# Kernel optimization log

Measured on AMD Instinct MI355X. Metric: run time of the kernel, lower is better.

Reference implementation:

```python
import jax, jax.numpy as jnp
import numpy as np

IOU_THR = 0.7
SCORE_THR = 0.01
KEEP_TOPK = 300
B, N, C = 16, 2048, 80


def box_cxcywh_to_xyxy(b):
    cx, cy, w, h = b[..., 0], b[..., 1], b[..., 2], b[..., 3]
    return jnp.stack([cx - 0.5 * w, cy - 0.5 * h, cx + 0.5 * w, cy + 0.5 * h], axis=-1)


def _iou_matrix(b):
    # b: [N,4] xyxy -> [N,N] IoU
    area = (b[:, 2] - b[:, 0]) * (b[:, 3] - b[:, 1])
    lt = jnp.maximum(b[:, None, :2], b[None, :, :2])
    rb = jnp.minimum(b[:, None, 2:], b[None, :, 2:])
    wh = jnp.clip(rb - lt, 0.0)
    inter = wh[..., 0] * wh[..., 1]
    union = area[:, None] + area[None, :] - inter
    return jnp.where(union > 0, inter / union, 0.0)


def _nms_image(boxes, scores, labels):
    # boxes [N,4], scores [N], labels [N] -> padded (labels [K], boxes [K,4], scores [K])
    n = boxes.shape[0]
    s = jnp.where(scores > SCORE_THR, scores, -1.0)
    order = jnp.argsort(-s)  # descending score, thresholded-out last
    b = boxes[order]
    sc = s[order]
    lb = labels[order]
    keep0 = sc > SCORE_THR
    # batched_nms trick: offset boxes per class so different classes never overlap
    offset = lb.astype(boxes.dtype) * (jnp.max(boxes) + 1.0)
    iou = _iou_matrix(b + offset[:, None])  # [N,N]
    idxs = jnp.arange(n)

    def body(i, keep):
        sup = keep[i] & (iou[i] > IOU_THR) & (idxs > i)
        return keep & ~sup

    keep = jax.lax.fori_loop(0, n, body, keep0)
    # first KEEP_TOPK kept boxes in score order; pad invalid slots
    sel = jnp.sort(jnp.where(keep, idxs, n))[:KEEP_TOPK]
    ok = sel < n
    sel_c = jnp.minimum(sel, n - 1)
    out_b = jnp.where(ok[:, None], b[sel_c], 0.0)
    out_s = jnp.where(ok, sc[sel_c], 0.0)
    out_l = jnp.where(ok, lb[sel_c], -1)
    return out_l, out_b, out_s


def setup_inputs() -> dict:
    key = jax.random.key(0)
    k1, k2, k3 = jax.random.split(key, 3)
    pred_logits = jax.random.normal(k1, (B, N, C), dtype=jnp.float32)
    pred_boxes = jax.random.uniform(k2, (B, N, 4), dtype=jnp.float32)  # normalized cxcywh
    orig_target_sizes = 480.0 + 800.0 * jax.random.uniform(k3, (B, 2), dtype=jnp.float32)
    return {"pred_logits": pred_logits, "pred_boxes": pred_boxes,
            "orig_target_sizes": orig_target_sizes}


def reference(pred_logits, pred_boxes, orig_target_sizes):
    boxes = box_cxcywh_to_xyxy(pred_boxes)  # [B,N,4]
    scale = jnp.tile(orig_target_sizes, (1, 2))[:, None, :]  # [B,1,4] = (w,h,w,h)
    boxes = boxes * scale
    vals = jnp.max(pred_logits, axis=-1)
    labels = jnp.argmax(pred_logits, axis=-1)
    scores = jax.nn.sigmoid(vals)
    out_l, out_b, out_s = jax.vmap(_nms_image)(boxes, scores, labels)
    return out_l, out_b, out_s
```

## Files before the change

### kernel.cpp

```cpp
#include <hip/hip_runtime.h>


#define NTHREADS 1024
constexpr int Bn = 16;
constexpr int Nn = 2048;
constexpr int Cc = 80;
constexpr int Kk = 300;
constexpr int CCAP = 64;
constexpr double IOU_THR = 0.7;
constexpr double SCORE_THR = 0.01;

__device__ unsigned long long g_keys[Bn * Nn];
__device__ unsigned long long g_skeys[Bn * Nn];
__device__ unsigned char g_lab[Bn * Nn];
__device__ unsigned short g_clp[Bn * Cc * CCAP];
__device__ unsigned short g_cloi[Bn * Cc * CCAP];
__device__ int g_ccnt[Bn * Cc];
__device__ unsigned int g_keepw[Bn * (Nn / 32)];

__global__ __launch_bounds__(256) void argmax_kernel(const float* __restrict__ logits)
{
    int gid = blockIdx.x * 256 + threadIdx.x;
    if (gid >= Bn * Nn) return;
    const float4* lp = (const float4*)(logits + (size_t)gid * Cc);
    float m = -__builtin_inff();
    int am = 0;
#pragma unroll
    for (int c = 0; c < Cc / 4; ++c) {
        float4 v = lp[c];
        if (v.x > m) { m = v.x; am = 4 * c + 0; }
        if (v.y > m) { m = v.y; am = 4 * c + 1; }
        if (v.z > m) { m = v.z; am = 4 * c + 2; }
        if (v.w > m) { m = v.w; am = 4 * c + 3; }
    }
    unsigned mb = __float_as_uint(m);
    unsigned asc = mb ^ ((mb & 0x80000000u) ? 0xFFFFFFFFu : 0x80000000u);
    unsigned n = (unsigned)(gid & (Nn - 1));
    g_keys[gid] = ((unsigned long long)(~asc) << 32) | n;
    g_lab[gid] = (unsigned char)am;
}

__device__ __forceinline__ void cx(unsigned long long& a, unsigned long long p, bool takeMin)
{
    bool aless = a < p;
    a = (takeMin == aless) ? a : p;
}

__launch_bounds__(NTHREADS, 1)
__global__ void sort_compact_kernel()
{
    __shared__ unsigned long long dbuf[2][Nn];
    __shared__ unsigned int hist[32 * Cc];
    __shared__ int s_nv;
    const int t = threadIdx.x;
    const int b = blockIdx.x;
    const size_t base = (size_t)b * Nn;

    if (t == 0) s_nv = 0;
    if (t < Nn / 32) g_keepw[b * (Nn / 32) + t] = 0u;
    for (int i = t; i < 32 * Cc; i += NTHREADS) hist[i] = 0u;

    unsigned long long v0 = g_keys[base + t];
    unsigned long long v1 = g_keys[base + t + 1024];

    {
        int vc = 0;
#pragma unroll
        for (int e = 0; e < 2; ++e) {
            unsigned hi = (unsigned)((e ? v1 : v0) >> 32);
            unsigned ascb = ~hi;
            unsigned mb = (ascb & 0x80000000u) ? (ascb ^ 0x80000000u) : ~ascb;
            float m = __uint_as_float(mb);
            double sd = 1.0 / (1.0 + exp(-(double)m));
            if (sd > SCORE_THR) vc++;
        }
        for (int off = 32; off > 0; off >>= 1) vc += __shfl_down(vc, off);
        if ((t & 63) == 0) atomicAdd(&s_nv, vc);
    }

    int cur = 0;
    for (int k = 2; k <= Nn; k <<= 1) {
        for (int j = k >> 1; j > 0; j >>= 1) {
            if (j >= 1024) {
                unsigned long long mn = (v0 < v1) ? v0 : v1;
                unsigned long long mx = (v0 < v1) ? v1 : v0;
                v0 = mn; v1 = mx;
            } else if (j >= 64) {
                dbuf[cur][t] = v0;
                dbuf[cur][t + 1024] = v1;
                __syncthreads();
                unsigned long long p0 = dbuf[cur][t ^ j];
                unsigned long long p1 = dbuf[cur][(t ^ j) + 1024];
                bool lower = ((t & j) == 0);
                cx(v0, p0, lower == ((t & k) == 0));
                cx(v1, p1, lower == (((t + 1024) & k) == 0));
                cur ^= 1;
            } else {
                unsigned long long p0 = __shfl_xor(v0, j);
                unsigned long long p1 = __shfl_xor(v1, j);
                bool lower = ((t & j) == 0);
                cx(v0, p0, lower == ((t & k) == 0));
                cx(v1, p1, lower == (((t + 1024) & k) == 0));
            }
        }
    }
    const int nv = s_nv;

    const int oi0 = (int)(v0 & 0xFFFFu);
    const int oi1 = (int)(v1 & 0xFFFFu);
    const int c0 = (t < nv) ? (int)g_lab[base + oi0] : 127;
    const int c1 = (t + 1024 < nv) ? (int)g_lab[base + oi1] : 127;
    if (c0 < 127) atomicAdd(&hist[(t >> 6) * Cc + c0], 1u);
    if (c1 < 127) atomicAdd(&hist[((t + 1024) >> 6) * Cc + c1], 1u);
    g_skeys[base + t] = v0;
    g_skeys[base + t + 1024] = v1;
    __syncthreads();

    if (t < Cc) {
        unsigned run = 0;
        for (int ch = 0; ch < 32; ++ch) {
            unsigned v = hist[ch * Cc + t];
            hist[ch * Cc + t] = run;
            run += v;
        }
        g_ccnt[b * Cc + t] = (int)((run < CCAP) ? run : CCAP);
    }
    __syncthreads();

    const int l = t & 63;
    const unsigned long long below = (l == 0) ? 0ull : ((1ull << l) - 1ull);
#pragma unroll
    for (int e = 0; e < 2; ++e) {
        const int p = e ? (t + 1024) : t;
        const int c7 = e ? c1 : c0;
        const int oi = e ? oi1 : oi0;
        unsigned long long mm = ~0ull;
#pragma unroll
        for (int bit = 0; bit < 7; ++bit) {
            unsigned long long vote = __ballot((c7 >> bit) & 1);
            mm &= ((c7 >> bit) & 1) ? vote : ~vote;
        }
        if (c7 < 127) {
            int r = (int)hist[(p >> 6) * Cc + c7] + __popcll(mm & below);
            if (r < CCAP) {
                g_clp[((size_t)b * Cc + c7) * CCAP + r] = (unsigned short)p;
                g_cloi[((size_t)b * Cc + c7) * CCAP + r] = (unsigned short)oi;
            }
        }
    }
}

__launch_bounds__(64, 8)
__global__ void pairnms_kernel(const float* __restrict__ pboxes,
                               const float* __restrict__ osize)
{
    __shared__ double lb[CCAP][5];
    const int bc = blockIdx.x;
    const int b = bc / Cc;
    const int j = threadIdx.x;
    const int cnt = g_ccnt[bc];
    if (cnt == 0) return;
    const double s0 = (double)osize[2 * b + 0];
    const double s1 = (double)osize[2 * b + 1];

    unsigned short p = 0;
    double jx1 = 0, jy1 = 0, jx2 = 0, jy2 = 0, aj = 0;
    if (j < cnt) {
        p = g_clp[(size_t)bc * CCAP + j];
        int oi = g_cloi[(size_t)bc * CCAP + j];
        const float* bp = pboxes + ((size_t)b * Nn + oi) * 4;
        double cx = (double)bp[0], cy = (double)bp[1];
        double w  = (double)bp[2], h  = (double)bp[3];
        jx1 = (cx - 0.5 * w) * s0; jy1 = (cy - 0.5 * h) * s1;
        jx2 = (cx + 0.5 * w) * s0; jy2 = (cy + 0.5 * h) * s1;
        aj = (jx2 - jx1) * (jy2 - jy1);
        lb[j][0] = jx1; lb[j][1] = jy1; lb[j][2] = jx2; lb[j][3] = jy2; lb[j][4] = aj;
    }
    __syncthreads();

    unsigned long long mymask = 0ull;
    if (j < cnt) {
        for (int i = 0; i < j; ++i) {
            double lt0 = fmax(lb[i][0], jx1), lt1 = fmax(lb[i][1], jy1);
            double rb0 = fmin(lb[i][2], jx2), rb1 = fmin(lb[i][3], jy2);
            double w0 = fmax(rb0 - lt0, 0.0), w1 = fmax(rb1 - lt1, 0.0);
            double inter = w0 * w1;
            double uni = lb[i][4] + aj - inter;
            if (uni > 0.0 && inter > IOU_THR * uni) mymask |= 1ull << i;
        }
    }

    unsigned long long K = 0ull;
    for (int r = 0; r < cnt; ++r) {
        unsigned long long mr = __shfl(mymask, r);
        if ((mr & K) == 0ull) K |= 1ull << r;
    }
    if (j < cnt && ((K >> j) & 1ull))
        atomicOr(&g_keepw[b * (Nn / 32) + (p >> 5)], 1u << (p & 31));
}

#define FT 512
__launch_bounds__(FT, 1)
__global__ void finalize_kernel(const float* __restrict__ pboxes,
                                const float* __restrict__ osize,
                                float* __restrict__ out)
{
    __shared__ unsigned int kw[Nn / 32];
    __shared__ int kpre[Nn / 32];
    __shared__ int out_posS[Kk];
    __shared__ int s_kept;
    const int t = threadIdx.x;
    const int b = blockIdx.x;
    const double s0 = (double)osize[2 * b + 0];
    const double s1 = (double)osize[2 * b + 1];

    if (t < Nn / 32) kw[t] = g_keepw[b * (Nn / 32) + t];
    __syncthreads();
    if (t < 64) {
        unsigned w = kw[t];
        int pc = __popc(w);
        int inc = pc;
        for (int off = 1; off < 64; off <<= 1) {
            int v = __shfl_up(inc, off);
            if (t >= off) inc += v;
        }
        kpre[t] = inc - pc;
        if (t == 63) s_kept = (inc < Kk) ? inc : Kk;
    }
    __syncthreads();
    for (int p = t; p < Nn; p += FT) {
        if ((kw[p >> 5] >> (p & 31)) & 1u) {
            int rank = kpre[p >> 5] + __popc(kw[p >> 5] & ((1u << (p & 31)) - 1u));
            if (rank < Kk) out_posS[rank] = p;
        }
    }
    __syncthreads();

    const int kept = s_kept;
    const int base_b = Bn * Kk;
    const int base_s = Bn * Kk * 5;
    for (int r = t; r < Kk; r += FT) {
        float lf = -1.0f, b0 = 0.f, b1 = 0.f, b2 = 0.f, b3 = 0.f, sf = 0.f;
        if (r < kept) {
            int p = out_posS[r];
            unsigned long long kk = g_skeys[(size_t)b * Nn + p];
            unsigned oi = (unsigned)(kk & 0xFFFFu);
            lf = (float)g_lab[(size_t)b * Nn + oi];
            unsigned hi = (unsigned)(kk >> 32);
            unsigned ascb = ~hi;
            unsigned mb = (ascb & 0x80000000u) ? (ascb ^ 0x80000000u) : ~ascb;
            float m = __uint_as_float(mb);
            sf = (float)(1.0 / (1.0 + exp(-(double)m)));
            const float* bp = pboxes + ((size_t)b * Nn + oi) * 4;
            double cx = (double)bp[0], cy = (double)bp[1];
            double w  = (double)bp[2], h  = (double)bp[3];
            b0 = (float)((cx - 0.5 * w) * s0);
            b1 = (float)((cy - 0.5 * h) * s1);
            b2 = (float)((cx + 0.5 * w) * s0);
            b3 = (float)((cy + 0.5 * h) * s1);
        }
        out[b * Kk + r] = lf;
        float* ob = out + base_b + (size_t)(b * Kk + r) * 4;
        ob[0] = b0; ob[1] = b1; ob[2] = b2; ob[3] = b3;
        out[base_s + b * Kk + r] = sf;
    }
}

extern "C" void kernel_launch(void* const* d_in, const int* in_sizes, int n_in,
                              void* d_out, int out_size, void* d_ws, size_t ws_size,
                              hipStream_t stream)
{
    const float* logits = (const float*)d_in[0];
    const float* pboxes = (const float*)d_in[1];
    const float* osize  = (const float*)d_in[2];
    float* out = (float*)d_out;
    argmax_kernel<<<(Bn * Nn + 255) / 256, 256, 0, stream>>>(logits);
    sort_compact_kernel<<<Bn, NTHREADS, 0, stream>>>();
    pairnms_kernel<<<Bn * Cc, 64, 0, stream>>>(pboxes, osize);
    finalize_kernel<<<Bn, FT, 0, stream>>>(pboxes, osize, out);
}
```

Before: 42.33 us.

## Fuse argmax into sort kernel and finalize into NMS via last-block counter

The argmax over logits moves into the per-image sort kernel, so keys no longer round-trip through global memory. The finalize step is merged into the per-class NMS kernel: each block bumps a per-image done counter, and the last block to finish compacts the kept boxes and writes the outputs. This cuts four launches to two. The cost is that the argmax now runs on only 16 blocks of 1024 threads, which may limit memory bandwidth on 10.5 MB of logits, and the finalize work runs on a single 64-thread block per image.

```diff
diff --git a/kernel.cpp b/kernel.cpp
--- a/kernel.cpp
+++ b/kernel.cpp
@@ -10,35 +10,13 @@
 constexpr double IOU_THR = 0.7;
 constexpr double SCORE_THR = 0.01;
 
-__device__ unsigned long long g_keys[Bn * Nn];
 __device__ unsigned long long g_skeys[Bn * Nn];
 __device__ unsigned char g_lab[Bn * Nn];
 __device__ unsigned short g_clp[Bn * Cc * CCAP];
 __device__ unsigned short g_cloi[Bn * Cc * CCAP];
 __device__ int g_ccnt[Bn * Cc];
 __device__ unsigned int g_keepw[Bn * (Nn / 32)];
-
-__global__ __launch_bounds__(256) void argmax_kernel(const float* __restrict__ logits)
-{
-    int gid = blockIdx.x * 256 + threadIdx.x;
-    if (gid >= Bn * Nn) return;
-    const float4* lp = (const float4*)(logits + (size_t)gid * Cc);
-    float m = -__builtin_inff();
-    int am = 0;
-#pragma unroll
-    for (int c = 0; c < Cc / 4; ++c) {
-        float4 v = lp[c];
-        if (v.x > m) { m = v.x; am = 4 * c + 0; }
-        if (v.y > m) { m = v.y; am = 4 * c + 1; }
-        if (v.z > m) { m = v.z; am = 4 * c + 2; }
-        if (v.w > m) { m = v.w; am = 4 * c + 3; }
-    }
-    unsigned mb = __float_as_uint(m);
-    unsigned asc = mb ^ ((mb & 0x80000000u) ? 0xFFFFFFFFu : 0x80000000u);
-    unsigned n = (unsigned)(gid & (Nn - 1));
-    g_keys[gid] = ((unsigned long long)(~asc) << 32) | n;
-    g_lab[gid] = (unsigned char)am;
-}
+__device__ unsigned int g_done[Bn];
 
 __device__ __forceinline__ void cx(unsigned long long& a, unsigned long long p, bool takeMin)
 {
@@ -47,7 +25,7 @@
 }
 
 __launch_bounds__(NTHREADS, 1)
-__global__ void sort_compact_kernel()
+__global__ void prep_kernel(const float* __restrict__ logits)
 {
     __shared__ unsigned long long dbuf[2][Nn];
     __shared__ unsigned int hist[32 * Cc];
@@ -56,27 +34,36 @@
     const int b = blockIdx.x;
     const size_t base = (size_t)b * Nn;
 
-    if (t == 0) s_nv = 0;
+    if (t == 0) { s_nv = 0; g_done[b] = 0u; }
     if (t < Nn / 32) g_keepw[b * (Nn / 32) + t] = 0u;
     for (int i = t; i < 32 * Cc; i += NTHREADS) hist[i] = 0u;
 
-    unsigned long long v0 = g_keys[base + t];
-    unsigned long long v1 = g_keys[base + t + 1024];
-
-    {
-        int vc = 0;
-#pragma unroll
-        for (int e = 0; e < 2; ++e) {
-            unsigned hi = (unsigned)((e ? v1 : v0) >> 32);
-            unsigned ascb = ~hi;
-            unsigned mb = (ascb & 0x80000000u) ? (ascb ^ 0x80000000u) : ~ascb;
-            float m = __uint_as_float(mb);
-            double sd = 1.0 / (1.0 + exp(-(double)m));
-            if (sd > SCORE_THR) vc++;
-        }
-        for (int off = 32; off > 0; off >>= 1) vc += __shfl_down(vc, off);
-        if ((t & 63) == 0) atomicAdd(&s_nv, vc);
-    }
+    unsigned long long v0, v1;
+    int vc = 0;
+#pragma unroll
+    for (int e = 0; e < 2; ++e) {
+        const int n = t + (e << 10);
+        const float4* lp = (const float4*)(logits + (base + n) * Cc);
+        float m = -__builtin_inff();
+        int am = 0;
+#pragma unroll
+        for (int c = 0; c < Cc / 4; ++c) {
+            float4 v = lp[c];
+            if (v.x > m) { m = v.x; am = 4 * c + 0; }
+            if (v.y > m) { m = v.y; am = 4 * c + 1; }
+            if (v.z > m) { m = v.z; am = 4 * c + 2; }
+            if (v.w > m) { m = v.w; am = 4 * c + 3; }
+        }
+        unsigned mb = __float_as_uint(m);
+        unsigned asc = mb ^ ((mb & 0x80000000u) ? 0xFFFFFFFFu : 0x80000000u);
+        unsigned long long key = ((unsigned long long)(~asc) << 32) | (unsigned)n;
+        if (e) v1 = key; else v0 = key;
+        g_lab[base + n] = (unsigned char)am;
+        double sd = 1.0 / (1.0 + exp(-(double)m));
+        if (sd > SCORE_THR) vc++;
+    }
+    for (int off = 32; off > 0; off >>= 1) vc += __shfl_down(vc, off);
+    if ((t & 63) == 0) atomicAdd(&s_nv, vc);
 
     int cur = 0;
     for (int k = 2; k <= Nn; k <<= 1) {
@@ -151,73 +138,73 @@
 }
 
 __launch_bounds__(64, 8)
-__global__ void pairnms_kernel(const float* __restrict__ pboxes,
-                               const float* __restrict__ osize)
+__global__ void nms_finalize_kernel(const float* __restrict__ pboxes,
+                                    const float* __restrict__ osize,
+                                    float* __restrict__ out)
 {
     __shared__ double lb[CCAP][5];
-    const int bc = blockIdx.x;
-    const int b = bc / Cc;
-    const int j = threadIdx.x;
-    const int cnt = g_ccnt[bc];
-    if (cnt == 0) return;
-    const double s0 = (double)osize[2 * b + 0];
-    const double s1 = (double)osize[2 * b + 1];
-
-    unsigned short p = 0;
-    double jx1 = 0, jy1 = 0, jx2 = 0, jy2 = 0, aj = 0;
-    if (j < cnt) {
-        p = g_clp[(size_t)bc * CCAP + j];
-        int oi = g_cloi[(size_t)bc * CCAP + j];
-        const float* bp = pboxes + ((size_t)b * Nn + oi) * 4;
-        double cx = (double)bp[0], cy = (double)bp[1];
-        double w  = (double)bp[2], h  = (double)bp[3];
-        jx1 = (cx - 0.5 * w) * s0; jy1 = (cy - 0.5 * h) * s1;
-        jx2 = (cx + 0.5 * w) * s0; jy2 = (cy + 0.5 * h) * s1;
-        aj = (jx2 - jx1) * (jy2 - jy1);
-        lb[j][0] = jx1; lb[j][1] = jy1; lb[j][2] = jx2; lb[j][3] = jy2; lb[j][4] = aj;
-    }
-    __syncthreads();
-
-    unsigned long long mymask = 0ull;
-    if (j < cnt) {
-        for (int i = 0; i < j; ++i) {
-            double lt0 = fmax(lb[i][0], jx1), lt1 = fmax(lb[i][1], jy1);
-            double rb0 = fmin(lb[i][2], jx2), rb1 = fmin(lb[i][3], jy2);
-            double w0 = fmax(rb0 - lt0, 0.0), w1 = fmax(rb1 - lt1, 0.0);
-            double inter = w0 * w1;
-            double uni = lb[i][4] + aj - inter;
-            if (uni > 0.0 && inter > IOU_THR * uni) mymask |= 1ull << i;
-        }
-    }
-
-    unsigned long long K = 0ull;
-    for (int r = 0; r < cnt; ++r) {
-        unsigned long long mr = __shfl(mymask, r);
-        if ((mr & K) == 0ull) K |= 1ull << r;
-    }
-    if (j < cnt && ((K >> j) & 1ull))
-        atomicOr(&g_keepw[b * (Nn / 32) + (p >> 5)], 1u << (p & 31));
-}
-
-#define FT 512
-__launch_bounds__(FT, 1)
-__global__ void finalize_kernel(const float* __restrict__ pboxes,
-                                const float* __restrict__ osize,
-                                float* __restrict__ out)
-{
     __shared__ unsigned int kw[Nn / 32];
     __shared__ int kpre[Nn / 32];
     __shared__ int out_posS[Kk];
     __shared__ int s_kept;
+    __shared__ int s_last;
+
+    const int bc = blockIdx.x;
+    const int b = bc / Cc;
     const int t = threadIdx.x;
-    const int b = blockIdx.x;
+    const int cnt = g_ccnt[bc];
     const double s0 = (double)osize[2 * b + 0];
     const double s1 = (double)osize[2 * b + 1];
 
-    if (t < Nn / 32) kw[t] = g_keepw[b * (Nn / 32) + t];
-    __syncthreads();
-    if (t < 64) {
-        unsigned w = kw[t];
+    if (cnt > 0) {
+        const int j = t;
+        unsigned short p = 0;
+        double jx1 = 0, jy1 = 0, jx2 = 0, jy2 = 0, aj = 0;
+        if (j < cnt) {
+            p = g_clp[(size_t)bc * CCAP + j];
+            int oi = g_cloi[(size_t)bc * CCAP + j];
+            const float* bp = pboxes + ((size_t)b * Nn + oi) * 4;
+            double cx = (double)bp[0], cy = (double)bp[1];
+            double w  = (double)bp[2], h  = (double)bp[3];
+            jx1 = (cx - 0.5 * w) * s0; jy1 = (cy - 0.5 * h) * s1;
+            jx2 = (cx + 0.5 * w) * s0; jy2 = (cy + 0.5 * h) * s1;
+            aj = (jx2 - jx1) * (jy2 - jy1);
+            lb[j][0] = jx1; lb[j][1] = jy1; lb[j][2] = jx2; lb[j][3] = jy2; lb[j][4] = aj;
+        }
+        __syncthreads();
+
+        unsigned long long mymask = 0ull;
+        if (j < cnt) {
+            for (int i = 0; i < j; ++i) {
+                double lt0 = fmax(lb[i][0], jx1), lt1 = fmax(lb[i][1], jy1);
+                double rb0 = fmin(lb[i][2], jx2), rb1 = fmin(lb[i][3], jy2);
+                double w0 = fmax(rb0 - lt0, 0.0), w1 = fmax(rb1 - lt1, 0.0);
+                double inter = w0 * w1;
+                double uni = lb[i][4] + aj - inter;
+                if (uni > 0.0 && inter > IOU_THR * uni) mymask |= 1ull << i;
+            }
+        }
+        unsigned long long K = 0ull;
+        for (int r = 0; r < cnt; ++r) {
+            unsigned long long mr = __shfl(mymask, r);
+            if ((mr & K) == 0ull) K |= 1ull << r;
+        }
+        if (j < cnt && ((K >> j) & 1ull))
+            atomicOr(&g_keepw[b * (Nn / 32) + (p >> 5)], 1u << (p & 31));
+    }
+
+    __syncthreads();
+    if (t == 0) {
+        __threadfence();
+        unsigned old = atomicAdd(&g_done[b], 1u);
+        s_last = (old == (unsigned)(Cc - 1)) ? 1 : 0;
+    }
+    __syncthreads();
+    if (!s_last) return;
+
+    {
+        unsigned w = atomicAdd(&g_keepw[b * (Nn / 32) + t], 0u);
+        kw[t] = w;
         int pc = __popc(w);
         int inc = pc;
         for (int off = 1; off < 64; off <<= 1) {
@@ -228,7 +215,7 @@
         if (t == 63) s_kept = (inc < Kk) ? inc : Kk;
     }
     __syncthreads();
-    for (int p = t; p < Nn; p += FT) {
+    for (int p = t; p < Nn; p += 64) {
         if ((kw[p >> 5] >> (p & 31)) & 1u) {
             int rank = kpre[p >> 5] + __popc(kw[p >> 5] & ((1u << (p & 31)) - 1u));
             if (rank < Kk) out_posS[rank] = p;
@@ -239,7 +226,7 @@
     const int kept = s_kept;
     const int base_b = Bn * Kk;
     const int base_s = Bn * Kk * 5;
-    for (int r = t; r < Kk; r += FT) {
+    for (int r = t; r < Kk; r += 64) {
         float lf = -1.0f, b0 = 0.f, b1 = 0.f, b2 = 0.f, b3 = 0.f, sf = 0.f;
         if (r < kept) {
             int p = out_posS[r];
@@ -274,8 +261,6 @@
     const float* pboxes = (const float*)d_in[1];
     const float* osize  = (const float*)d_in[2];
     float* out = (float*)d_out;
-    argmax_kernel<<<(Bn * Nn + 255) / 256, 256, 0, stream>>>(logits);
-    sort_compact_kernel<<<Bn, NTHREADS, 0, stream>>>();
-    pairnms_kernel<<<Bn * Cc, 64, 0, stream>>>(pboxes, osize);
-    finalize_kernel<<<Bn, FT, 0, stream>>>(pboxes, osize, out);
-}
+    prep_kernel<<<Bn, NTHREADS, 0, stream>>>(logits);
+    nms_finalize_kernel<<<Bn * Cc, 64, 0, stream>>>(pboxes, osize, out);
+}
```

After: 64.92 us. 53.4% more time.
